# Performance work log

Measured on AMD Instinct MI355X. Metric: run time of the kernel, lower is better.

The kernel has to match this reference:

```python
import jax, jax.numpy as jnp
import numpy as np

D_MODEL = 1024
NUM_HEADS = 16
HEAD_DIM = D_MODEL // NUM_HEADS
SCALE = HEAD_DIM ** -0.5
LN_EPS = 1e-5
Q_EPS = 1e-5


def bit_quant(W):
    # BitNet b1.58 ternary weight quantization with straight-through estimator.
    gamma = jnp.mean(jnp.abs(W))
    Wq = jnp.clip(jnp.round(W / (gamma + Q_EPS)), -1.0, 1.0) * gamma
    return W + jax.lax.stop_gradient(Wq - W)


def layer_norm(x, gamma, beta):
    mu = jnp.mean(x, axis=-1, keepdims=True)
    var = jnp.mean(jnp.square(x - mu), axis=-1, keepdims=True)
    return (x - mu) * jax.lax.rsqrt(var + LN_EPS) * gamma + beta


def setup_inputs() -> dict:
    key = jax.random.key(0)
    ks = jax.random.split(key, 8)
    B, T, T_ctx, C = 4, 1024, 2048, D_MODEL
    w_std = C ** -0.5
    return {
        "x": jax.random.normal(ks[0], (B, T, C), jnp.float32),
        "context": jax.random.normal(ks[1], (B, T_ctx, C), jnp.float32),
        "Wq": jax.random.normal(ks[2], (C, C), jnp.float32) * w_std,
        "bq": jnp.zeros((C,), jnp.float32),
        "Wk": jax.random.normal(ks[3], (C, C), jnp.float32) * w_std,
        "bk": jnp.zeros((C,), jnp.float32),
        "Wv": jax.random.normal(ks[4], (C, C), jnp.float32) * w_std,
        "bv": jnp.zeros((C,), jnp.float32),
        "Wo": jax.random.normal(ks[5], (C, C), jnp.float32) * w_std,
        "bo": jnp.zeros((C,), jnp.float32),
        "ln_gamma": jnp.ones((C,), jnp.float32),
        "ln_beta": jnp.zeros((C,), jnp.float32),
    }


def reference(x, context, Wq, bq, Wk, bk, Wv, bv, Wo, bo, ln_gamma, ln_beta):
    B, T, C = x.shape
    T_ctx = context.shape[1]
    residual = x
    xn = layer_norm(x, ln_gamma, ln_beta)
    # BitNet-quantized projections (torch Linear: y = x @ W.T + b)
    q = xn @ bit_quant(Wq).T + bq                      # [B,T,C]
    k = context @ bit_quant(Wk).T + bk                 # [B,T_ctx,C]
    v = context @ bit_quant(Wv).T + bv                 # [B,T_ctx,C]
    q = q.reshape(B, T, NUM_HEADS, HEAD_DIM)
    k = k.reshape(B, T_ctx, NUM_HEADS, HEAD_DIM)
    v = v.reshape(B, T_ctx, NUM_HEADS, HEAD_DIM)
    scores = jnp.einsum("bqhd,bkhd->bhqk", q, k) * SCALE   # [B,H,T,T_ctx]
    probs = jax.nn.softmax(scores, axis=-1)
    out = jnp.einsum("bhqk,bkhd->bqhd", probs, v).reshape(B, T, C)
    return residual + (out @ bit_quant(Wo).T + bo)
```

## Files before the change

kernel.cpp:

```cpp
#include <hip/hip_runtime.h>
#include <hip/hip_bf16.h>

typedef __attribute__((ext_vector_type(8))) short s8x;
typedef __attribute__((ext_vector_type(4))) float f4x;
typedef unsigned short u16;
typedef unsigned int u32;

#define T_ 1024
#define TC_ 2048
#define SCLOG2E 0.1803368801111243f

#define WAIT_VM(n) asm volatile("s_waitcnt vmcnt(" #n ")" ::: "memory")

__device__ __forceinline__ u16 f2bf(float f) {
    u32 u = __float_as_uint(f);
    return (u16)((u + 0x7fffu + ((u >> 16) & 1u)) >> 16);
}

#if defined(__has_builtin)
#if __has_builtin(__builtin_amdgcn_cvt_pk_bf16_f32)
#define HAVE_PK 1
#endif
#if __has_builtin(__builtin_amdgcn_permlane16_swap) && __has_builtin(__builtin_amdgcn_permlane32_swap)
#define HAVE_PLSWAP 1
#endif
#endif

__device__ __forceinline__ u32 pack2bf(float a, float b) {
#ifdef HAVE_PK
    typedef __attribute__((ext_vector_type(2))) __bf16 bf2t;
    bf2t r = __builtin_amdgcn_cvt_pk_bf16_f32(a, b);
    u32 u;
    __builtin_memcpy(&u, &r, 4);
    return u;
#else
    return (u32)f2bf(a) | ((u32)f2bf(b) << 16);
#endif
}

__device__ __forceinline__ void pswap32(u32& a, u32& b) {
#ifdef HAVE_PLSWAP
    typedef __attribute__((ext_vector_type(2))) unsigned int u2x;
    u2x r = __builtin_amdgcn_permlane32_swap(a, b, false, false);
    a = r.x; b = r.y;
#else
    asm("v_permlane32_swap_b32 %0, %1" : "+v"(a), "+v"(b));
#endif
}
__device__ __forceinline__ void pswap16(u32& a, u32& b) {
#ifdef HAVE_PLSWAP
    typedef __attribute__((ext_vector_type(2))) unsigned int u2x;
    u2x r = __builtin_amdgcn_permlane16_swap(a, b, false, false);
    a = r.x; b = r.y;
#else
    asm("v_permlane16_swap_b32 %0, %1" : "+v"(a), "+v"(b));
#endif
}

__device__ __forceinline__ void gload16(const void* g, void* l) {
    __builtin_amdgcn_global_load_lds((const __attribute__((address_space(1))) u32*)g,
                                     (__attribute__((address_space(3))) u32*)l, 16, 0, 0);
}

__global__ __launch_bounds__(256) void absmean_k(const float* __restrict__ W0, const float* __restrict__ W1,
                                                 const float* __restrict__ W2, const float* __restrict__ W3,
                                                 float* __restrict__ gsum) {
    int wi = blockIdx.y;
    const float* W = (wi == 0) ? W0 : (wi == 1) ? W1 : (wi == 2) ? W2 : W3;
    const int n4 = (1024 * 1024) / 4;
    float s = 0.f;
    int stride = gridDim.x * blockDim.x;
    for (int i = blockIdx.x * blockDim.x + threadIdx.x; i < n4; i += stride) {
        float4 v = ((const float4*)W)[i];
        s += fabsf(v.x) + fabsf(v.y) + fabsf(v.z) + fabsf(v.w);
    }
#pragma unroll
    for (int off = 32; off; off >>= 1) s += __shfl_down(s, off, 64);
    __shared__ float ps[4];
    if ((threadIdx.x & 63) == 0) ps[threadIdx.x >> 6] = s;
    __syncthreads();
    if (threadIdx.x == 0) atomicAdd(gsum + wi, ps[0] + ps[1] + ps[2] + ps[3]);
}

__global__ __launch_bounds__(256) void prep_k(
        const float* __restrict__ x, const float* __restrict__ lng, const float* __restrict__ lnb,
        u16* __restrict__ xn,
        const float* __restrict__ ctx, u16* __restrict__ ctxb,
        const float* __restrict__ W0, const float* __restrict__ W1,
        const float* __restrict__ W2, const float* __restrict__ W3,
        u16* __restrict__ D0, u16* __restrict__ D1, u16* __restrict__ D2, u16* __restrict__ D3,
        const float* __restrict__ gsum) {
    __shared__ float ps[8];
    int bx = blockIdx.x, t = threadIdx.x;
    if (bx < 4096) {
        int row = bx;
        float4 xv = ((const float4*)(x + (long)row * 1024))[t];
        float s = xv.x + xv.y + xv.z + xv.w;
        float s2 = xv.x * xv.x + xv.y * xv.y + xv.z * xv.z + xv.w * xv.w;
#pragma unroll
        for (int off = 32; off; off >>= 1) { s += __shfl_down(s, off, 64); s2 += __shfl_down(s2, off, 64); }
        if ((t & 63) == 0) { ps[t >> 6] = s; ps[4 + (t >> 6)] = s2; }
        __syncthreads();
        float S = ps[0] + ps[1] + ps[2] + ps[3];
        float S2 = ps[4] + ps[5] + ps[6] + ps[7];
        float mu = S * (1.f / 1024.f);
        float var = S2 * (1.f / 1024.f) - mu * mu;
        float rstd = rsqrtf(var + 1e-5f);
        float4 gv = ((const float4*)lng)[t];
        float4 bv = ((const float4*)lnb)[t];
        uint2 o;
        o.x = pack2bf((xv.x - mu) * rstd * gv.x + bv.x, (xv.y - mu) * rstd * gv.y + bv.y);
        o.y = pack2bf((xv.z - mu) * rstd * gv.z + bv.z, (xv.w - mu) * rstd * gv.w + bv.w);
        ((uint2*)(xn + (long)row * 1024))[t] = o;
    } else if (bx < 12288) {
        int i = (bx - 4096) * 256 + t;
        float4 v = ((const float4*)ctx)[i];
        uint2 o = {pack2bf(v.x, v.y), pack2bf(v.z, v.w)};
        ((uint2*)ctxb)[i] = o;
    } else {
        int wi = (bx - 12288) >> 10;
        const float* W = (wi == 0) ? W0 : (wi == 1) ? W1 : (wi == 2) ? W2 : W3;
        u16* D = (wi == 0) ? D0 : (wi == 1) ? D1 : (wi == 2) ? D2 : D3;
        float inv = 1.0f / (gsum[wi] * (1.0f / 1048576.0f) + 1e-5f);
        int i = ((bx - 12288) & 1023) * 256 + t;
        float4 wv = ((const float4*)W)[i];
        uint2 o;
        o.x = pack2bf(fminf(1.f, fmaxf(-1.f, rintf(wv.x * inv))),
                      fminf(1.f, fmaxf(-1.f, rintf(wv.y * inv))));
        o.y = pack2bf(fminf(1.f, fmaxf(-1.f, rintf(wv.z * inv))),
                      fminf(1.f, fmaxf(-1.f, rintf(wv.w * inv))));
        ((uint2*)D)[i] = o;
    }
}

__global__ __launch_bounds__(256) void gemm_fused(
        const u16* __restrict__ xn, const u16* __restrict__ ctxb,
        const u16* __restrict__ wtq, const u16* __restrict__ wtk, const u16* __restrict__ wtv,
        const float* __restrict__ bq, const float* __restrict__ bk, const float* __restrict__ bv,
        const float* __restrict__ gsum,
        u16* __restrict__ qb, u16* __restrict__ kb, u16* __restrict__ vtb) {
    __shared__ __align__(16) char smem[65536];
    int tid = threadIdx.x;
    int w = tid >> 6, l = tid & 63, lq = l & 15, lh = l >> 4;
    int wm = (w >> 1) * 64, wn = (w & 1) * 64;
    int bx = blockIdx.x;
    int xcd = bx & 7;
    int prob, m0, n0, gidx;
    const u16 *A, *Wt;
    const float* bias;
    float sc;
    if (bx < 256) {
        int local = bx >> 3;
        prob = 0; A = xn; Wt = wtq; bias = bq; sc = SCLOG2E; gidx = 0;
        m0 = (xcd * 4 + (local & 3)) * 128;
        n0 = (local >> 2) * 128;
    } else {
        int b = bx - 256;
        int local3 = b >> 3;
        int kv = local3 & 1;
        int idx = local3 >> 1;
        prob = 1 + kv; A = ctxb;
        Wt = kv ? wtv : wtk; bias = kv ? bv : bk; sc = 1.0f; gidx = 1 + kv;
        m0 = (xcd * 8 + (idx & 7)) * 128;
        n0 = (idx >> 3) * 128;
    }
    int sp = tid >> 3, ss = tid & 7;
    int st = ss ^ (sp & 7);
    int r0 = sp * 2 + (st >> 2), c0 = st & 3;
    const u16* Ag0 = A + (long)(m0 + r0) * 1024 + c0 * 8;
    const u16* Ag1 = Ag0 + 64 * 1024;
    const u16* Bg0 = Wt + (long)(n0 + r0) * 1024 + c0 * 8;
    const u16* Bg1 = Bg0 + 64 * 1024;
    int aoff[4], boff[4];
#pragma unroll
    for (int i = 0; i < 4; i++) {
        int ar = wm + i * 16 + lq, ap = ar >> 1;
        aoff[i] = ap * 128 + (((((ar & 1) << 2) | lh) ^ (ap & 7)) * 16);
        int br = wn + i * 16 + lq, bp = br >> 1;
        boff[i] = bp * 128 + (((((br & 1) << 2) | lh) ^ (bp & 7)) * 16);
    }
    f4x acc[4][4] = {};
#define STAGE_G(kt, buf)                                                   \
    {                                                                      \
        char* Ad = smem + (buf) * 32768;                                   \
        gload16(Ag0 + (kt) * 64, Ad + tid * 16);                           \
        gload16(Ag1 + (kt) * 64, Ad + 4096 + tid * 16);                    \
        gload16(Ag0 + (kt) * 64 + 32, Ad + 8192 + tid * 16);               \
        gload16(Ag1 + (kt) * 64 + 32, Ad + 12288 + tid * 16);              \
        gload16(Bg0 + (kt) * 64, Ad + 16384 + tid * 16);                   \
        gload16(Bg1 + (kt) * 64, Ad + 20480 + tid * 16);                   \
        gload16(Bg0 + (kt) * 64 + 32, Ad + 24576 + tid * 16);              \
        gload16(Bg1 + (kt) * 64 + 32, Ad + 28672 + tid * 16);              \
    }
    STAGE_G(0, 0);
    STAGE_G(1, 1);
#pragma unroll
    for (int kt = 0; kt < 16; kt++) {
        if (kt < 15) { WAIT_VM(8); } else { WAIT_VM(0); }
        __builtin_amdgcn_s_barrier();
        const char* Ac = smem + (kt & 1) * 32768;
        const char* Bc = Ac + 16384;
        s8x af[2][4], bfr[2][4];
#pragma unroll
        for (int h = 0; h < 2; h++)
#pragma unroll
            for (int i = 0; i < 4; i++) {
                af[h][i] = *(const s8x*)(Ac + h * 8192 + aoff[i]);
                bfr[h][i] = *(const s8x*)(Bc + h * 8192 + boff[i]);
            }
#pragma unroll
        for (int h = 0; h < 2; h++)
#pragma unroll
            for (int i = 0; i < 4; i++)
#pragma unroll
                for (int j = 0; j < 4; j++)
                    acc[i][j] = __builtin_amdgcn_mfma_f32_16x16x32_bf16(af[h][i], bfr[h][j], acc[i][j], 0, 0, 0);
        __builtin_amdgcn_s_barrier();
        if (kt + 2 < 16) STAGE_G(kt + 2, kt & 1);
    }
    float gamma = gsum[gidx] * (1.0f / 1048576.0f) * sc;
    if (prob < 2) {
        u16* outq = (prob == 0) ? qb : kb;
        int tshift = (prob == 0) ? 10 : 11;
        int tmask = (1 << tshift) - 1;
#pragma unroll
        for (int i = 0; i < 4; i++) {
            int gr = m0 + wm + i * 16 + lh * 4;
#pragma unroll
            for (int j = 0; j < 4; j++) {
                int gc = n0 + wn + j * 16 + lq;
                float bb = bias[gc] * sc;
                int h = gc >> 6, d = gc & 63;
#pragma unroll
                for (int r = 0; r < 4; r++) {
                    int row = gr + r;
                    int bidx = row >> tshift, tt = row & tmask;
                    outq[((((long)(bidx * 16 + h)) << tshift) + tt) * 64 + d] = f2bf(acc[i][j][r] * gamma + bb);
                }
            }
        }
    } else {
        __syncthreads();
        char* Ct = smem;
#pragma unroll
        for (int i = 0; i < 4; i++) {
            int tt = wm + i * 16 + lh * 4;
#pragma unroll
            for (int j = 0; j < 4; j++) {
                int c = wn + j * 16 + lq;
                float bb = bias[n0 + c];
                uint2 pk;
                pk.x = pack2bf(acc[i][j][0] * gamma + bb, acc[i][j][1] * gamma + bb);
                pk.y = pack2bf(acc[i][j][2] * gamma + bb, acc[i][j][3] * gamma + bb);
                int slot = (tt >> 3) ^ (c & 15);
                *(uint2*)(Ct + c * 256 + slot * 16 + (tt & 7) * 2) = pk;
            }
        }
        __syncthreads();
        int bb2 = m0 >> 11, t0 = m0 & 2047;
#pragma unroll
        for (int it = 0; it < 8; it++) {
            int e = it * 256 + tid;
            int c = e >> 4, ch = e & 15;
            int slot = ch ^ (c & 15);
            s8x v = *(const s8x*)(Ct + c * 256 + slot * 16);
            int gcg = n0 + c;
            int h = gcg >> 6, d = gcg & 63;
            *(s8x*)(vtb + ((long)((bb2 * 16 + h) * 64 + d)) * TC_ + t0 + ch * 8) = v;
        }
    }
}

__global__ __launch_bounds__(256) void gemm_o(const u16* __restrict__ A, const u16* __restrict__ Wt,
                                              const float* __restrict__ bias, const float* __restrict__ gsum,
                                              const float* __restrict__ residual, float* __restrict__ outr) {
    __shared__ __align__(16) char smem[49152];
    int tid = threadIdx.x;
    int w = tid >> 6, l = tid & 63, lq = l & 15, lh = l >> 4;
    int wm = (w >> 1) * 64, wn = (w & 1) * 32;
    int bx = blockIdx.x;
    int xcd = bx & 7, local = bx >> 3;
    int m0 = (xcd * 4 + (local & 3)) * 128;
    int n0 = (local >> 2) * 64;
    int sp = tid >> 3, ss = tid & 7;
    int st = ss ^ (sp & 7);
    int r0 = sp * 2 + (st >> 2), c0 = st & 3;
    const u16* Ag0 = A + (long)(m0 + r0) * 1024 + c0 * 8;
    const u16* Ag1 = Ag0 + 64 * 1024;
    const u16* Bg0 = Wt + (long)(n0 + r0) * 1024 + c0 * 8;
    int aoff[4], boff[2];
#pragma unroll
    for (int i = 0; i < 4; i++) {
        int ar = wm + i * 16 + lq, ap = ar >> 1;
        aoff[i] = ap * 128 + (((((ar & 1) << 2) | lh) ^ (ap & 7)) * 16);
    }
#pragma unroll
    for (int j = 0; j < 2; j++) {
        int br = wn + j * 16 + lq, bp = br >> 1;
        boff[j] = bp * 128 + (((((br & 1) << 2) | lh) ^ (bp & 7)) * 16);
    }
    f4x acc[4][2] = {};
#define STAGE_O(kt, buf)                                                   \
    {                                                                      \
        char* Ad = smem + (buf) * 24576;                                   \
        gload16(Ag0 + (kt) * 64, Ad + tid * 16);                           \
        gload16(Ag1 + (kt) * 64, Ad + 4096 + tid * 16);                    \
        gload16(Ag0 + (kt) * 64 + 32, Ad + 8192 + tid * 16);               \
        gload16(Ag1 + (kt) * 64 + 32, Ad + 12288 + tid * 16);              \
        gload16(Bg0 + (kt) * 64, Ad + 16384 + tid * 16);                   \
        gload16(Bg0 + (kt) * 64 + 32, Ad + 20480 + tid * 16);              \
    }
    STAGE_O(0, 0);
    STAGE_O(1, 1);
#pragma unroll
    for (int kt = 0; kt < 16; kt++) {
        if (kt < 15) { WAIT_VM(6); } else { WAIT_VM(0); }
        __builtin_amdgcn_s_barrier();
        const char* Ac = smem + (kt & 1) * 24576;
        const char* Bc = Ac + 16384;
        s8x af[2][4], bfr[2][2];
#pragma unroll
        for (int h = 0; h < 2; h++) {
#pragma unroll
            for (int i = 0; i < 4; i++) af[h][i] = *(const s8x*)(Ac + h * 8192 + aoff[i]);
#pragma unroll
            for (int j = 0; j < 2; j++) bfr[h][j] = *(const s8x*)(Bc + h * 4096 + boff[j]);
        }
#pragma unroll
        for (int h = 0; h < 2; h++)
#pragma unroll
            for (int i = 0; i < 4; i++)
#pragma unroll
                for (int j = 0; j < 2; j++)
                    acc[i][j] = __builtin_amdgcn_mfma_f32_16x16x32_bf16(af[h][i], bfr[h][j], acc[i][j], 0, 0, 0);
        __builtin_amdgcn_s_barrier();
        if (kt + 2 < 16) STAGE_O(kt + 2, kt & 1);
    }
    float gamma = gsum[3] * (1.0f / 1048576.0f);
#pragma unroll
    for (int i = 0; i < 4; i++) {
        int gr = m0 + wm + i * 16 + lh * 4;
#pragma unroll
        for (int j = 0; j < 2; j++) {
            int gc = n0 + wn + j * 16 + lq;
            float bb = bias[gc];
#pragma unroll
            for (int r = 0; r < 4; r++) {
                long idx = (long)(gr + r) * 1024 + gc;
                outr[idx] = residual[idx] + acc[i][j][r] * gamma + bb;
            }
        }
    }
}

__global__ __launch_bounds__(256, 2) void attn_k(const u16* __restrict__ qh, const u16* __restrict__ kh,
                                                 const u16* __restrict__ vth, u16* __restrict__ attn) {
    __shared__ __align__(16) char smem[49152];
    int tid = threadIdx.x, w = tid >> 6, l = tid & 63, lq = l & 15, lh = l >> 4;
    int bh = blockIdx.x, q0 = blockIdx.y * 128;
    const u16* qp = qh + ((long)bh * T_ + q0) * 64;
#pragma unroll
    for (int i = 0; i < 4; i++) {
        int cid = i * 256 + tid;
        int r = cid >> 3, c = (cid & 7) ^ (r & 7);
        gload16(qp + r * 64 + c * 8, smem + cid * 16);
    }
    __syncthreads();
    s8x qf[2][2];
#pragma unroll
    for (int qb = 0; qb < 2; qb++)
#pragma unroll
        for (int dh = 0; dh < 2; dh++) {
            int qrow = w * 32 + qb * 16 + lq;
            int ch = (dh * 4 + lh) ^ (qrow & 7);
            qf[qb][dh] = *(const s8x*)(smem + qrow * 128 + ch * 16);
        }
    __syncthreads();
    int sr = tid >> 3, sc = (tid & 7) ^ ((tid >> 3) & 7);
    const u16* kgA = kh + (long)bh * TC_ * 64 + sr * 64 + sc * 8;
    const u16* kgB = kgA + 2048;
    const u16* vgA = vth + (long)bh * 64 * TC_ + (long)sr * TC_ + sc * 8;
    const u16* vgB = vgA + 32 * TC_;
    const char* pA = smem + lq * 128 + ((lh ^ (lq & 7)) * 16);
    const char* pB = smem + lq * 128 + (((4 + lh) ^ (lq & 7)) * 16);
#define STAGE3(buf)                                              \
    {                                                            \
        char* Kb = smem + (buf) * 16384;                         \
        gload16(kgA, Kb + tid * 16);                             \
        gload16(kgB, Kb + 4096 + tid * 16);                      \
        gload16(vgA, Kb + 8192 + tid * 16);                      \
        gload16(vgB, Kb + 12288 + tid * 16);                     \
        kgA += 4096; kgB += 4096; vgA += 64; vgB += 64;          \
    }
#define SM1(ZA, qb, PF0, PF1)                                                                              \
    s8x PF0, PF1;                                                                                          \
    {                                                                                                      \
        u32 w00 = pack2bf(__builtin_amdgcn_exp2f(ZA[qb][0][0]), __builtin_amdgcn_exp2f(ZA[qb][0][1]));     \
        u32 w01 = pack2bf(__builtin_amdgcn_exp2f(ZA[qb][0][2]), __builtin_amdgcn_exp2f(ZA[qb][0][3]));     \
        u32 w10 = pack2bf(__builtin_amdgcn_exp2f(ZA[qb][1][0]), __builtin_amdgcn_exp2f(ZA[qb][1][1]));     \
        u32 w11 = pack2bf(__builtin_amdgcn_exp2f(ZA[qb][1][2]), __builtin_amdgcn_exp2f(ZA[qb][1][3]));     \
        u32 w20 = pack2bf(__builtin_amdgcn_exp2f(ZA[qb][2][0]), __builtin_amdgcn_exp2f(ZA[qb][2][1]));     \
        u32 w21 = pack2bf(__builtin_amdgcn_exp2f(ZA[qb][2][2]), __builtin_amdgcn_exp2f(ZA[qb][2][3]));     \
        u32 w30 = pack2bf(__builtin_amdgcn_exp2f(ZA[qb][3][0]), __builtin_amdgcn_exp2f(ZA[qb][3][1]));     \
        u32 w31 = pack2bf(__builtin_amdgcn_exp2f(ZA[qb][3][2]), __builtin_amdgcn_exp2f(ZA[qb][3][3]));     \
        u32 a0w = w00, a1w = w10; pswap32(a0w, a1w); pswap16(a0w, a1w);                                    \
        u32 b0w = w01, b1w = w11; pswap32(b0w, b1w); pswap16(b0w, b1w);                                    \
        u32 c0w = w20, c1w = w30; pswap32(c0w, c1w); pswap16(c0w, c1w);                                    \
        u32 d0w = w21, d1w = w31; pswap32(d0w, d1w); pswap16(d0w, d1w);                                    \
        u32 pw0[4] = {a0w, b0w, a1w, b1w};                                                                 \
        u32 pw1[4] = {c0w, d0w, c1w, d1w};                                                                 \
        __builtin_memcpy(&PF0, pw0, 16);                                                                   \
        __builtin_memcpy(&PF1, pw1, 16);                                                                   \
    }
#define SUBITER(JB, KB, SB, ZC, ZN, DOSTAGE)                                                               \
    {                                                                                                      \
        WAIT_VM(0);                                                                                        \
        __builtin_amdgcn_s_barrier();                                                                      \
        if (DOSTAGE) STAGE3(SB);                                                                           \
        s8x a0_[4], a1_[4], v0_[4], v1_[4];                                                                \
        _Pragma("unroll") for (int ni = 0; ni < 4; ni++) {                                                 \
            a0_[ni] = *(const s8x*)(pA + (KB) * 16384 + ni * 2048);                                        \
            a1_[ni] = *(const s8x*)(pB + (KB) * 16384 + ni * 2048);                                        \
        }                                                                                                  \
        _Pragma("unroll") for (int nd = 0; nd < 4; nd++) {                                                 \
            v0_[nd] = *(const s8x*)(pA + (JB) * 16384 + 8192 + nd * 2048);                                 \
            v1_[nd] = *(const s8x*)(pB + (JB) * 16384 + 8192 + nd * 2048);                                 \
        }                                                                                                  \
        SM1(ZC, 0, pfa0, pfa1)                                                                             \
        __builtin_amdgcn_s_setprio(1);                                                                     \
        _Pragma("unroll") for (int ni = 0; ni < 4; ni++) {                                                 \
            _Pragma("unroll") for (int qb = 0; qb < 2; qb++) {                                             \
                f4x zz = {0.f, 0.f, 0.f, 0.f};                                                             \
                zz = __builtin_amdgcn_mfma_f32_16x16x32_bf16(a0_[ni], qf[qb][0], zz, 0, 0, 0);             \
                zz = __builtin_amdgcn_mfma_f32_16x16x32_bf16(a1_[ni], qf[qb][1], zz, 0, 0, 0);             \
                ZN[qb][ni] = zz;                                                                           \
            }                                                                                              \
        }                                                                                                  \
        __builtin_amdgcn_s_setprio(0);                                                                     \
        SM1(ZC, 1, pfb0, pfb1)                                                                             \
        __builtin_amdgcn_s_setprio(1);                                                                     \
        lrun[0] = __builtin_amdgcn_mfma_f32_16x16x32_bf16(pfa0, ones, lrun[0], 0, 0, 0);                   \
        lrun[0] = __builtin_amdgcn_mfma_f32_16x16x32_bf16(pfa1, ones, lrun[0], 0, 0, 0);                   \
        lrun[1] = __builtin_amdgcn_mfma_f32_16x16x32_bf16(pfb0, ones, lrun[1], 0, 0, 0);                   \
        lrun[1] = __builtin_amdgcn_mfma_f32_16x16x32_bf16(pfb1, ones, lrun[1], 0, 0, 0);                   \
        _Pragma("unroll") for (int nd = 0; nd < 4; nd++) {                                                 \
            oacc[0][nd] = __builtin_amdgcn_mfma_f32_16x16x32_bf16(pfa0, v0_[nd], oacc[0][nd], 0, 0, 0);    \
            oacc[0][nd] = __builtin_amdgcn_mfma_f32_16x16x32_bf16(pfa1, v1_[nd], oacc[0][nd], 0, 0, 0);    \
            oacc[1][nd] = __builtin_amdgcn_mfma_f32_16x16x32_bf16(pfb0, v0_[nd], oacc[1][nd], 0, 0, 0);    \
            oacc[1][nd] = __builtin_amdgcn_mfma_f32_16x16x32_bf16(pfb1, v1_[nd], oacc[1][nd], 0, 0, 0);    \
        }                                                                                                  \
        __builtin_amdgcn_s_setprio(0);                                                                     \
    }
    const s8x ones = {16256, 16256, 16256, 16256, 16256, 16256, 16256, 16256};
    f4x z0[2][4], z1[2][4];
    f4x oacc[2][4] = {};
    f4x lrun[2] = {};
    STAGE3(0); STAGE3(1);
    WAIT_VM(4);
    __builtin_amdgcn_s_barrier();
    {
        s8x a0_[4], a1_[4];
#pragma unroll
        for (int ni = 0; ni < 4; ni++) {
            a0_[ni] = *(const s8x*)(pA + ni * 2048);
            a1_[ni] = *(const s8x*)(pB + ni * 2048);
        }
#pragma unroll
        for (int ni = 0; ni < 4; ni++)
#pragma unroll
            for (int qb = 0; qb < 2; qb++) {
                f4x zz = {0.f, 0.f, 0.f, 0.f};
                zz = __builtin_amdgcn_mfma_f32_16x16x32_bf16(a0_[ni], qf[qb][0], zz, 0, 0, 0);
                zz = __builtin_amdgcn_mfma_f32_16x16x32_bf16(a1_[ni], qf[qb][1], zz, 0, 0, 0);
                z0[qb][ni] = zz;
            }
    }
    for (int t = 0; t < 5; t++) {
        SUBITER(0, 1, 2, z0, z1, true)
        SUBITER(1, 2, 0, z1, z0, true)
        SUBITER(2, 0, 1, z0, z1, true)
        SUBITER(0, 1, 2, z1, z0, true)
        SUBITER(1, 2, 0, z0, z1, true)
        SUBITER(2, 0, 1, z1, z0, true)
    }
    SUBITER(0, 1, 2, z0, z1, false)
    {
        s8x v0_[4], v1_[4];
#pragma unroll
        for (int nd = 0; nd < 4; nd++) {
            v0_[nd] = *(const s8x*)(pA + 1 * 16384 + 8192 + nd * 2048);
            v1_[nd] = *(const s8x*)(pB + 1 * 16384 + 8192 + nd * 2048);
        }
        SM1(z1, 0, pfa0, pfa1)
        SM1(z1, 1, pfb0, pfb1)
        __builtin_amdgcn_s_setprio(1);
        lrun[0] = __builtin_amdgcn_mfma_f32_16x16x32_bf16(pfa0, ones, lrun[0], 0, 0, 0);
        lrun[0] = __builtin_amdgcn_mfma_f32_16x16x32_bf16(pfa1, ones, lrun[0], 0, 0, 0);
        lrun[1] = __builtin_amdgcn_mfma_f32_16x16x32_bf16(pfb0, ones, lrun[1], 0, 0, 0);
        lrun[1] = __builtin_amdgcn_mfma_f32_16x16x32_bf16(pfb1, ones, lrun[1], 0, 0, 0);
#pragma unroll
        for (int nd = 0; nd < 4; nd++) {
            oacc[0][nd] = __builtin_amdgcn_mfma_f32_16x16x32_bf16(pfa0, v0_[nd], oacc[0][nd], 0, 0, 0);
            oacc[0][nd] = __builtin_amdgcn_mfma_f32_16x16x32_bf16(pfa1, v1_[nd], oacc[0][nd], 0, 0, 0);
            oacc[1][nd] = __builtin_amdgcn_mfma_f32_16x16x32_bf16(pfb0, v0_[nd], oacc[1][nd], 0, 0, 0);
            oacc[1][nd] = __builtin_amdgcn_mfma_f32_16x16x32_bf16(pfb1, v1_[nd], oacc[1][nd], 0, 0, 0);
        }
        __builtin_amdgcn_s_setprio(0);
    }
    int b = bh >> 4, h = bh & 15;
#pragma unroll
    for (int qb = 0; qb < 2; qb++)
#pragma unroll
        for (int r = 0; r < 4; r++) {
            int q = q0 + w * 32 + qb * 16 + lh * 4 + r;
            float rcp = 1.f / lrun[qb][r];
#pragma unroll
            for (int nd = 0; nd < 4; nd++)
                attn[((long)(b * T_ + q)) * 1024 + h * 64 + nd * 16 + lq] = f2bf(oacc[qb][nd][r] * rcp);
        }
}

extern "C" void kernel_launch(void* const* d_in, const int* in_sizes, int n_in,
                              void* d_out, int out_size, void* d_ws, size_t ws_size,
                              hipStream_t stream) {
    const float* x   = (const float*)d_in[0];
    const float* ctx = (const float*)d_in[1];
    const float* Wq  = (const float*)d_in[2];
    const float* bq  = (const float*)d_in[3];
    const float* Wk  = (const float*)d_in[4];
    const float* bk  = (const float*)d_in[5];
    const float* Wv  = (const float*)d_in[6];
    const float* bv  = (const float*)d_in[7];
    const float* Wo  = (const float*)d_in[8];
    const float* bo  = (const float*)d_in[9];
    const float* lng = (const float*)d_in[10];
    const float* lnb = (const float*)d_in[11];
    float* out = (float*)d_out;

    char* ws = (char*)d_ws;
    float* gsum = (float*)ws;
    size_t off = 256;
    u16* wtq  = (u16*)(ws + off); off += (size_t)1024 * 1024 * 2;
    u16* wtk  = (u16*)(ws + off); off += (size_t)1024 * 1024 * 2;
    u16* wtv  = (u16*)(ws + off); off += (size_t)1024 * 1024 * 2;
    u16* wto  = (u16*)(ws + off); off += (size_t)1024 * 1024 * 2;
    u16* ctxb = (u16*)(ws + off); off += (size_t)8192 * 1024 * 2;
    u16* xn   = (u16*)(ws + off); off += (size_t)4096 * 1024 * 2;
    u16* qb_  = (u16*)(ws + off); off += (size_t)4096 * 1024 * 2;
    u16* kb   = (u16*)(ws + off); off += (size_t)8192 * 1024 * 2;
    u16* vtb  = (u16*)(ws + off); off += (size_t)8192 * 1024 * 2;
    u16* attnb = xn;

    hipMemsetAsync(gsum, 0, 16, stream);
    absmean_k<<<dim3(128, 4), 256, 0, stream>>>(Wq, Wk, Wv, Wo, gsum);
    prep_k<<<16384, 256, 0, stream>>>(x, lng, lnb, xn, ctx, ctxb,
                                      Wq, Wk, Wv, Wo, wtq, wtk, wtv, wto, gsum);
    gemm_fused<<<1280, 256, 0, stream>>>(xn, ctxb, wtq, wtk, wtv, bq, bk, bv, gsum, qb_, kb, vtb);
    attn_k<<<dim3(64, 8), 256, 0, stream>>>(qb_, kb, vtb, attnb);
    gemm_o<<<512, 256, 0, stream>>>(attnb, wto, bo, gsum, x, out);
}
```

Measured before the change: 237.6 us.

## Halve attention query tile to 64 rows and double grid for occupancy

Each attention block now handles 64 query rows instead of 128: every wave owns one 16-row query block, not two. The grid doubles to 1024 blocks and launch bounds rise to 3 blocks per CU, since fewer accumulators and score registers are live. The aim is better CU occupancy and load balance. In exchange, every K/V tile is streamed from global memory twice as often, and each K/V load is reused over half as many MFMAs.

Result: slower. 242.9 us (+2.2%).

```diff
diff --git a/kernel.cpp b/kernel.cpp
--- a/kernel.cpp
+++ b/kernel.cpp
@@ -353,28 +353,26 @@
     }
 }
 
-__global__ __launch_bounds__(256, 2) void attn_k(const u16* __restrict__ qh, const u16* __restrict__ kh,
+__global__ __launch_bounds__(256, 3) void attn_k(const u16* __restrict__ qh, const u16* __restrict__ kh,
                                                  const u16* __restrict__ vth, u16* __restrict__ attn) {
     __shared__ __align__(16) char smem[49152];
     int tid = threadIdx.x, w = tid >> 6, l = tid & 63, lq = l & 15, lh = l >> 4;
-    int bh = blockIdx.x, q0 = blockIdx.y * 128;
+    int bh = blockIdx.x, q0 = blockIdx.y * 64;
     const u16* qp = qh + ((long)bh * T_ + q0) * 64;
 #pragma unroll
-    for (int i = 0; i < 4; i++) {
+    for (int i = 0; i < 2; i++) {
         int cid = i * 256 + tid;
         int r = cid >> 3, c = (cid & 7) ^ (r & 7);
         gload16(qp + r * 64 + c * 8, smem + cid * 16);
     }
     __syncthreads();
-    s8x qf[2][2];
-#pragma unroll
-    for (int qb = 0; qb < 2; qb++)
-#pragma unroll
-        for (int dh = 0; dh < 2; dh++) {
-            int qrow = w * 32 + qb * 16 + lq;
-            int ch = (dh * 4 + lh) ^ (qrow & 7);
-            qf[qb][dh] = *(const s8x*)(smem + qrow * 128 + ch * 16);
-        }
+    s8x qf[2];
+#pragma unroll
+    for (int dh = 0; dh < 2; dh++) {
+        int qrow = w * 16 + lq;
+        int ch = (dh * 4 + lh) ^ (qrow & 7);
+        qf[dh] = *(const s8x*)(smem + qrow * 128 + ch * 16);
+    }
     __syncthreads();
     int sr = tid >> 3, sc = (tid & 7) ^ ((tid >> 3) & 7);
     const u16* kgA = kh + (long)bh * TC_ * 64 + sr * 64 + sc * 8;
@@ -392,17 +390,17 @@
         gload16(vgB, Kb + 12288 + tid * 16);                     \
         kgA += 4096; kgB += 4096; vgA += 64; vgB += 64;          \
     }
-#define SM1(ZA, qb, PF0, PF1)                                                                              \
+#define SM1(ZA, PF0, PF1)                                                                                  \
     s8x PF0, PF1;                                                                                          \
     {                                                                                                      \
-        u32 w00 = pack2bf(__builtin_amdgcn_exp2f(ZA[qb][0][0]), __builtin_amdgcn_exp2f(ZA[qb][0][1]));     \
-        u32 w01 = pack2bf(__builtin_amdgcn_exp2f(ZA[qb][0][2]), __builtin_amdgcn_exp2f(ZA[qb][0][3]));     \
-        u32 w10 = pack2bf(__builtin_amdgcn_exp2f(ZA[qb][1][0]), __builtin_amdgcn_exp2f(ZA[qb][1][1]));     \
-        u32 w11 = pack2bf(__builtin_amdgcn_exp2f(ZA[qb][1][2]), __builtin_amdgcn_exp2f(ZA[qb][1][3]));     \
-        u32 w20 = pack2bf(__builtin_amdgcn_exp2f(ZA[qb][2][0]), __builtin_amdgcn_exp2f(ZA[qb][2][1]));     \
-        u32 w21 = pack2bf(__builtin_amdgcn_exp2f(ZA[qb][2][2]), __builtin_amdgcn_exp2f(ZA[qb][2][3]));     \
-        u32 w30 = pack2bf(__builtin_amdgcn_exp2f(ZA[qb][3][0]), __builtin_amdgcn_exp2f(ZA[qb][3][1]));     \
-        u32 w31 = pack2bf(__builtin_amdgcn_exp2f(ZA[qb][3][2]), __builtin_amdgcn_exp2f(ZA[qb][3][3]));     \
+        u32 w00 = pack2bf(__builtin_amdgcn_exp2f(ZA[0][0]), __builtin_amdgcn_exp2f(ZA[0][1]));             \
+        u32 w01 = pack2bf(__builtin_amdgcn_exp2f(ZA[0][2]), __builtin_amdgcn_exp2f(ZA[0][3]));             \
+        u32 w10 = pack2bf(__builtin_amdgcn_exp2f(ZA[1][0]), __builtin_amdgcn_exp2f(ZA[1][1]));             \
+        u32 w11 = pack2bf(__builtin_amdgcn_exp2f(ZA[1][2]), __builtin_amdgcn_exp2f(ZA[1][3]));             \
+        u32 w20 = pack2bf(__builtin_amdgcn_exp2f(ZA[2][0]), __builtin_amdgcn_exp2f(ZA[2][1]));             \
+        u32 w21 = pack2bf(__builtin_amdgcn_exp2f(ZA[2][2]), __builtin_amdgcn_exp2f(ZA[2][3]));             \
+        u32 w30 = pack2bf(__builtin_amdgcn_exp2f(ZA[3][0]), __builtin_amdgcn_exp2f(ZA[3][1]));             \
+        u32 w31 = pack2bf(__builtin_amdgcn_exp2f(ZA[3][2]), __builtin_amdgcn_exp2f(ZA[3][3]));             \
         u32 a0w = w00, a1w = w10; pswap32(a0w, a1w); pswap16(a0w, a1w);                                    \
         u32 b0w = w01, b1w = w11; pswap32(b0w, b1w); pswap16(b0w, b1w);                                    \
         u32 c0w = w20, c1w = w30; pswap32(c0w, c1w); pswap16(c0w, c1w);                                    \
@@ -426,54 +424,39 @@
             v0_[nd] = *(const s8x*)(pA + (JB) * 16384 + 8192 + nd * 2048);                                 \
             v1_[nd] = *(const s8x*)(pB + (JB) * 16384 + 8192 + nd * 2048);                                 \
         }                                                                                                  \
-        SM1(ZC, 0, pfa0, pfa1)                                                                             \
+        SM1(ZC, pf0, pf1)                                                                                  \
         __builtin_amdgcn_s_setprio(1);                                                                     \
         _Pragma("unroll") for (int ni = 0; ni < 4; ni++) {                                                 \
-            _Pragma("unroll") for (int qb = 0; qb < 2; qb++) {                                             \
-                f4x zz = {0.f, 0.f, 0.f, 0.f};                                                             \
-                zz = __builtin_amdgcn_mfma_f32_16x16x32_bf16(a0_[ni], qf[qb][0], zz, 0, 0, 0);             \
-                zz = __builtin_amdgcn_mfma_f32_16x16x32_bf16(a1_[ni], qf[qb][1], zz, 0, 0, 0);             \
-                ZN[qb][ni] = zz;                                                                           \
-            }                                                                                              \
+            f4x zz = {0.f, 0.f, 0.f, 0.f};                                                                 \
+            zz = __builtin_amdgcn_mfma_f32_16x16x32_bf16(a0_[ni], qf[0], zz, 0, 0, 0);                     \
+            zz = __builtin_amdgcn_mfma_f32_16x16x32_bf16(a1_[ni], qf[1], zz, 0, 0, 0);                     \
+            ZN[ni] = zz;                                                                                   \
+        }                                                                                                  \
+        lrun = __builtin_amdgcn_mfma_f32_16x16x32_bf16(pf0, ones, lrun, 0, 0, 0);                          \
+        lrun = __builtin_amdgcn_mfma_f32_16x16x32_bf16(pf1, ones, lrun, 0, 0, 0);                          \
+        _Pragma("unroll") for (int nd = 0; nd < 4; nd++) {                                                 \
+            oacc[nd] = __builtin_amdgcn_mfma_f32_16x16x32_bf16(pf0, v0_[nd], oacc[nd], 0, 0, 0);           \
+            oacc[nd] = __builtin_amdgcn_mfma_f32_16x16x32_bf16(pf1, v1_[nd], oacc[nd], 0, 0, 0);           \
         }                                                                                                  \
         __builtin_amdgcn_s_setprio(0);                                                                     \
-        SM1(ZC, 1, pfb0, pfb1)                                                                             \
-        __builtin_amdgcn_s_setprio(1);                                                                     \
-        lrun[0] = __builtin_amdgcn_mfma_f32_16x16x32_bf16(pfa0, ones, lrun[0], 0, 0, 0);                   \
-        lrun[0] = __builtin_amdgcn_mfma_f32_16x16x32_bf16(pfa1, ones, lrun[0], 0, 0, 0);                   \
-        lrun[1] = __builtin_amdgcn_mfma_f32_16x16x32_bf16(pfb0, ones, lrun[1], 0, 0, 0);                   \
-        lrun[1] = __builtin_amdgcn_mfma_f32_16x16x32_bf16(pfb1, ones, lrun[1], 0, 0, 0);                   \
-        _Pragma("unroll") for (int nd = 0; nd < 4; nd++) {                                                 \
-            oacc[0][nd] = __builtin_amdgcn_mfma_f32_16x16x32_bf16(pfa0, v0_[nd], oacc[0][nd], 0, 0, 0);    \
-            oacc[0][nd] = __builtin_amdgcn_mfma_f32_16x16x32_bf16(pfa1, v1_[nd], oacc[0][nd], 0, 0, 0);    \
-            oacc[1][nd] = __builtin_amdgcn_mfma_f32_16x16x32_bf16(pfb0, v0_[nd], oacc[1][nd], 0, 0, 0);    \
-            oacc[1][nd] = __builtin_amdgcn_mfma_f32_16x16x32_bf16(pfb1, v1_[nd], oacc[1][nd], 0, 0, 0);    \
-        }                                                                                                  \
-        __builtin_amdgcn_s_setprio(0);                                                                     \
     }
     const s8x ones = {16256, 16256, 16256, 16256, 16256, 16256, 16256, 16256};
-    f4x z0[2][4], z1[2][4];
-    f4x oacc[2][4] = {};
-    f4x lrun[2] = {};
+    f4x z0[4], z1[4];
+    f4x oacc[4] = {};
+    f4x lrun = {};
     STAGE3(0); STAGE3(1);
     WAIT_VM(4);
     __builtin_amdgcn_s_barrier();
     {
-        s8x a0_[4], a1_[4];
 #pragma unroll
         for (int ni = 0; ni < 4; ni++) {
-            a0_[ni] = *(const s8x*)(pA + ni * 2048);
-            a1_[ni] = *(const s8x*)(pB + ni * 2048);
-        }
-#pragma unroll
-        for (int ni = 0; ni < 4; ni++)
-#pragma unroll
-            for (int qb = 0; qb < 2; qb++) {
-                f4x zz = {0.f, 0.f, 0.f, 0.f};
-                zz = __builtin_amdgcn_mfma_f32_16x16x32_bf16(a0_[ni], qf[qb][0], zz, 0, 0, 0);
-                zz = __builtin_amdgcn_mfma_f32_16x16x32_bf16(a1_[ni], qf[qb][1], zz, 0, 0, 0);
-                z0[qb][ni] = zz;
-            }
+            s8x a0_ = *(const s8x*)(pA + ni * 2048);
+            s8x a1_ = *(const s8x*)(pB + ni * 2048);
+            f4x zz = {0.f, 0.f, 0.f, 0.f};
+            zz = __builtin_amdgcn_mfma_f32_16x16x32_bf16(a0_, qf[0], zz, 0, 0, 0);
+            zz = __builtin_amdgcn_mfma_f32_16x16x32_bf16(a1_, qf[1], zz, 0, 0, 0);
+            z0[ni] = zz;
+        }
     }
     for (int t = 0; t < 5; t++) {
         SUBITER(0, 1, 2, z0, z1, true)
@@ -491,33 +474,26 @@
             v0_[nd] = *(const s8x*)(pA + 1 * 16384 + 8192 + nd * 2048);
             v1_[nd] = *(const s8x*)(pB + 1 * 16384 + 8192 + nd * 2048);
         }
-        SM1(z1, 0, pfa0, pfa1)
-        SM1(z1, 1, pfb0, pfb1)
+        SM1(z1, pf0, pf1)
         __builtin_amdgcn_s_setprio(1);
-        lrun[0] = __builtin_amdgcn_mfma_f32_16x16x32_bf16(pfa0, ones, lrun[0], 0, 0, 0);
-        lrun[0] = __builtin_amdgcn_mfma_f32_16x16x32_bf16(pfa1, ones, lrun[0], 0, 0, 0);
-        lrun[1] = __builtin_amdgcn_mfma_f32_16x16x32_bf16(pfb0, ones, lrun[1], 0, 0, 0);
-        lrun[1] = __builtin_amdgcn_mfma_f32_16x16x32_bf16(pfb1, ones, lrun[1], 0, 0, 0);
+        lrun = __builtin_amdgcn_mfma_f32_16x16x32_bf16(pf0, ones, lrun, 0, 0, 0);
+        lrun = __builtin_amdgcn_mfma_f32_16x16x32_bf16(pf1, ones, lrun, 0, 0, 0);
 #pragma unroll
         for (int nd = 0; nd < 4; nd++) {
-            oacc[0][nd] = __builtin_amdgcn_mfma_f32_16x16x32_bf16(pfa0, v0_[nd], oacc[0][nd], 0, 0, 0);
-            oacc[0][nd] = __builtin_amdgcn_mfma_f32_16x16x32_bf16(pfa1, v1_[nd], oacc[0][nd], 0, 0, 0);
-            oacc[1][nd] = __builtin_amdgcn_mfma_f32_16x16x32_bf16(pfb0, v0_[nd], oacc[1][nd], 0, 0, 0);
-            oacc[1][nd] = __builtin_amdgcn_mfma_f32_16x16x32_bf16(pfb1, v1_[nd], oacc[1][nd], 0, 0, 0);
+            oacc[nd] = __builtin_amdgcn_mfma_f32_16x16x32_bf16(pf0, v0_[nd], oacc[nd], 0, 0, 0);
+            oacc[nd] = __builtin_amdgcn_mfma_f32_16x16x32_bf16(pf1, v1_[nd], oacc[nd], 0, 0, 0);
         }
         __builtin_amdgcn_s_setprio(0);
     }
     int b = bh >> 4, h = bh & 15;
 #pragma unroll
-    for (int qb = 0; qb < 2; qb++)
-#pragma unroll
-        for (int r = 0; r < 4; r++) {
-            int q = q0 + w * 32 + qb * 16 + lh * 4 + r;
-            float rcp = 1.f / lrun[qb][r];
-#pragma unroll
-            for (int nd = 0; nd < 4; nd++)
-                attn[((long)(b * T_ + q)) * 1024 + h * 64 + nd * 16 + lq] = f2bf(oacc[qb][nd][r] * rcp);
-        }
+    for (int r = 0; r < 4; r++) {
+        int q = q0 + w * 16 + lh * 4 + r;
+        float rcp = 1.f / lrun[r];
+#pragma unroll
+        for (int nd = 0; nd < 4; nd++)
+            attn[((long)(b * T_ + q)) * 1024 + h * 64 + nd * 16 + lq] = f2bf(oacc[nd][r] * rcp);
+    }
 }
 
 extern "C" void kernel_launch(void* const* d_in, const int* in_sizes, int n_in,
@@ -556,6 +532,6 @@
     prep_k<<<16384, 256, 0, stream>>>(x, lng, lnb, xn, ctx, ctxb,
                                       Wq, Wk, Wv, Wo, wtq, wtk, wtv, wto, gsum);
     gemm_fused<<<1280, 256, 0, stream>>>(xn, ctxb, wtq, wtk, wtv, bq, bk, bv, gsum, qb_, kb, vtb);
-    attn_k<<<dim3(64, 8), 256, 0, stream>>>(qb_, kb, vtb, attnb);
+    attn_k<<<dim3(64, 16), 256, 0, stream>>>(qb_, kb, vtb, attnb);
     gemm_o<<<512, 256, 0, stream>>>(attnb, wto, bo, gsum, x, out);
 }
```
